# Optimization experiments

Hardware: AMD Instinct MI355X
Metric: run time of the kernel (lower is better)

## Reference

```python
import jax, jax.numpy as jnp
import numpy as np

TILE = 16       # tile_size
R = 8           # search_radius
MAX_OFF = 8     # max initial offset magnitude used in setup
PAD = R + MAX_OFF  # padding so all gathers are in-bounds


def setup_inputs() -> dict:
    key = jax.random.key(0)
    k1, k2, k3 = jax.random.split(key, 3)
    B, C, H, W = 4, 3, 512, 512
    src = jax.random.normal(k1, (B, C, H, W), jnp.float32)
    dst = jax.random.normal(k2, (B, C, H, W), jnp.float32)
    offset = jax.random.randint(k3, (B, 2, H // TILE, W // TILE), 0, 9).astype(jnp.int32)
    return {"src": src, "dst": dst, "offset": offset}


def _gather_patches(img, rows, cols):
    # img: [C, Hp, Wp]; rows/cols: [nTH, nTW, K] -> [C, nTH, nTW, K, K]
    return img[:, rows[:, :, :, None], cols[:, :, None, :]]


def _tile_matching(src, dst, offset, tile=TILE, r=R, pad=PAD):
    B, C, H, W = src.shape
    nTH, nTW = H // tile, W // tile
    win = tile + 2 * r
    nD = 2 * r + 1

    dst_pad = jnp.pad(dst, ((0, 0), (0, 0), (pad, pad), (pad, pad)))
    off_y = offset[:, 0]  # [B, nTH, nTW]
    off_x = offset[:, 1]

    ti = (jnp.arange(nTH) * tile)  # tile origins (rows)
    tj = (jnp.arange(nTW) * tile)  # tile origins (cols)
    ar = jnp.arange(win)

    rows = ti[None, :, None, None] + off_y[..., None] + (pad - r) + ar
    cols = tj[None, None, :, None] + off_x[..., None] + (pad - r) + ar

    patches = jax.vmap(_gather_patches)(dst_pad, rows, cols)

    # Source tiles: [B, C, nTH, nTW, tile, tile]
    src_t = src.reshape(B, C, nTH, tile, nTW, tile).transpose(0, 1, 2, 4, 3, 5)

    def step(carry, d):
        best_c, best_i = carry
        dy, dx = d // nD, d % nD
        cand = jax.lax.dynamic_slice(
            patches, (0, 0, 0, 0, dy, dx), (B, C, nTH, nTW, tile, tile))
        cost = jnp.abs(cand - src_t).sum(axis=(1, 4, 5))  # SAD: [B, nTH, nTW]
        better = cost < best_c
        return (jnp.where(better, cost, best_c),
                jnp.where(better, d, best_i)), None

    init = (jnp.full((B, nTH, nTW), jnp.inf, src.dtype),
            jnp.zeros((B, nTH, nTW), jnp.int32))
    (best_c, best_i), _ = jax.lax.scan(step, init, jnp.arange(nD * nD, dtype=jnp.int32))

    dy = best_i // nD - r  # best displacement in [-r, r]
    dx = best_i % nD - r
    new_off = jnp.stack([off_y + dy, off_x + dx], axis=1)  # [B, 2, nTH, nTW]

    # Gather aligned dst tiles at refined offsets -> aligned image [B, C, H, W]
    art = jnp.arange(tile)
    rows2 = ti[None, :, None, None] + (off_y + dy)[..., None] + pad + art
    cols2 = tj[None, None, :, None] + (off_x + dx)[..., None] + pad + art
    aligned_t = jax.vmap(_gather_patches)(dst_pad, rows2, cols2)
    aligned = aligned_t.transpose(0, 1, 2, 4, 3, 5).reshape(B, C, H, W)
    return new_off, aligned


def reference(src, dst, offset):
    return _tile_matching(src, dst, offset)
```

## Files before the change

### kernel.cpp

```cpp
#include <hip/hip_runtime.h>

#define TILE 16
#define RR 8
#define ND 17
#define HH 512
#define WW 512
#define CC 3
#define BB 4
#define WROWS 32
#define WSTR 36
#define SSTR 20
#define BLK 256

typedef float f4a __attribute__((ext_vector_type(4), aligned(4)));
typedef unsigned long long u64;

template <int N>
__device__ __forceinline__ float shl_add(float x) {
    return x + __int_as_float(
        __builtin_amdgcn_update_dpp(0, __float_as_int(x), 0x100 + N, 0xF, 0xF, true));
}
template <int MASK>
__device__ __forceinline__ float swz_add(float x) {
    int y = __builtin_amdgcn_ds_swizzle(__float_as_int(x), (MASK << 10) | 0x1F);
    return x + __int_as_float(y);
}

__device__ __forceinline__ u64 sad_pass(const float* Wl, const float S[CC][8],
                                        int dy, int i, int h, int jg) {
    float acc[9];
    #pragma unroll
    for (int a = 0; a < 9; ++a) acc[a] = 0.f;
    #pragma unroll
    for (int c = 0; c < CC; ++c) {
        const int wb = c * (WROWS * WSTR) + (dy + i) * WSTR + 8 * (h + jg);
        f4a a0 = *(const f4a*)&Wl[wb + 0];
        f4a a1 = *(const f4a*)&Wl[wb + 4];
        f4a a2 = *(const f4a*)&Wl[wb + 8];
        f4a a3 = *(const f4a*)&Wl[wb + 12];
        float W16[16] = { a0.x, a0.y, a0.z, a0.w, a1.x, a1.y, a1.z, a1.w,
                          a2.x, a2.y, a2.z, a2.w, a3.x, a3.y, a3.z, a3.w };
        #pragma unroll
        for (int a = 0; a < 9; ++a) {
            float s0 = acc[a];
            #pragma unroll
            for (int jl = 0; jl < 8; ++jl)
                s0 += fabsf(W16[a + jl] - S[c][jl]);
            acc[a] = s0;
        }
    }
    #pragma unroll
    for (int a = 0; a < 9; ++a) {
        float x = acc[a];
        x = shl_add<2>(x);
        x = shl_add<4>(x);
        x = shl_add<8>(x);
        x = swz_add<16>(x);
        x += __shfl_xor(x, 32);
        acc[a] = x;
    }
    float bc = h ? acc[1] : acc[0];
    int   ba = h;
    #pragma unroll
    for (int a = 1; a < 9; ++a)
        if (a > h && acc[a] < bc) { bc = acc[a]; ba = a; }
    const unsigned d = (unsigned)(dy * ND + 8 * h + ba);
    u64 key = ((u64)__float_as_uint(bc) << 32) | d;
    u64 ok  = __shfl_xor(key, 1);
    return ok < key ? ok : key;
}

__global__ __launch_bounds__(BLK, 8) void tile_kernel(const float* __restrict__ src,
                                                      const float* __restrict__ dst,
                                                      const int* __restrict__ offset,
                                                      float* __restrict__ out) {
    __shared__ float Wl[CC * WROWS * WSTR];
    __shared__ float Sl[CC * TILE * SSTR];
    __shared__ u64   keyL[4];

    const int bid  = blockIdx.x;
    const int tile = ((bid & 7) << 9) | (bid >> 3);
    const int b  = tile >> 10;
    const int th = (tile >> 5) & 31;
    const int tw = tile & 31;
    const int ti = th * TILE, tj = tw * TILE;
    const int oy = offset[(b * 2 + 0) * 1024 + th * 32 + tw];
    const int ox = offset[(b * 2 + 1) * 1024 + th * 32 + tw];
    const int t  = threadIdx.x;

    const int gy0 = ti + oy - RR;
    const int gx0 = tj + ox - RR;
    for (int k = t; k < CC * WROWS * 8; k += BLK) {
        int c   = k >> 8;
        int rem = k & 255;
        int row = rem >> 3;
        int cc  = (rem & 7) << 2;
        int gy = gy0 + row;
        int gx = gx0 + cc;
        float4 v = make_float4(0.f, 0.f, 0.f, 0.f);
        if ((unsigned)gy < HH) {
            const float* p = dst + ((size_t)(b * CC + c) * HH + gy) * WW;
            if ((unsigned)gx <= WW - 4) {
                f4a u = *(const f4a*)(p + gx);
                v = make_float4(u.x, u.y, u.z, u.w);
            } else {
                float* ve = (float*)&v;
                #pragma unroll
                for (int e = 0; e < 4; ++e) {
                    int g = gx + e;
                    if ((unsigned)g < WW) ve[e] = p[g];
                }
            }
        }
        *(f4a*)&Wl[c * (WROWS * WSTR) + row * WSTR + cc] = *(f4a*)&v;
    }
    if (t < 192) {
        int k   = t;
        int c   = k >> 6;
        int rem = k & 63;
        int row = rem >> 2;
        int cc  = (rem & 3) << 2;
        f4a v = *(const f4a*)(src + ((size_t)(b * CC + c) * HH + ti + row) * WW + tj + cc);
        *(f4a*)&Sl[c * (TILE * SSTR) + row * SSTR + cc] = v;
    }
    __syncthreads();

    const int wv = t >> 6;
    const int l  = t & 63;
    const int h  = l & 1;
    const int jg = (l >> 1) & 1;
    const int i  = l >> 2;

    float S[CC][8];
    #pragma unroll
    for (int c = 0; c < CC; ++c) {
        const int sb = c * (TILE * SSTR) + i * SSTR + 8 * jg;
        f4a s0 = *(const f4a*)&Sl[sb];
        f4a s1 = *(const f4a*)&Sl[sb + 4];
        S[c][0]=s0.x; S[c][1]=s0.y; S[c][2]=s0.z; S[c][3]=s0.w;
        S[c][4]=s1.x; S[c][5]=s1.y; S[c][6]=s1.z; S[c][7]=s1.w;
    }

    u64 bestkey = sad_pass(Wl, S, wv, i, h, jg);
    #pragma unroll
    for (int p = 1; p < 4; ++p) {
        u64 k2 = sad_pass(Wl, S, wv + 4 * p, i, h, jg);
        if (k2 < bestkey) bestkey = k2;
    }
    if (wv == 0) {
        u64 k2 = sad_pass(Wl, S, 16, i, h, jg);
        if (k2 < bestkey) bestkey = k2;
    }
    if (l == 0) keyL[wv] = bestkey;
    __syncthreads();

    u64 wk = keyL[0];
    #pragma unroll
    for (int w = 1; w < 4; ++w) { u64 kw = keyL[w]; if (kw < wk) wk = kw; }
    const int d   = (int)(wk & 0xFFFFFFFFu);
    const int bdy = d / ND;
    const int bdx = d - bdy * ND;

    if (t == 0) out[(b * 2 + 0) * 1024 + th * 32 + tw] = (float)(oy + bdy - RR);
    if (t == 1) out[(b * 2 + 1) * 1024 + th * 32 + tw] = (float)(ox + bdx - RR);

    float* aligned = out + BB * 2 * 1024;
    if (t < 192) {
        const int c   = t >> 6;
        const int rem = t & 63;
        const int ii  = rem >> 2;
        const int jj4 = (rem & 3) << 2;
        const float* wp = &Wl[c * (WROWS * WSTR) + (bdy + ii) * WSTR + bdx + jj4];
        float4 v = make_float4(wp[0], wp[1], wp[2], wp[3]);
        *(f4a*)&aligned[((size_t)(b * CC + c) * HH + ti + ii) * WW + tj + jj4] =
            *(f4a*)&v;
    }
}

extern "C" void kernel_launch(void* const* d_in, const int* in_sizes, int n_in,
                              void* d_out, int out_size, void* d_ws, size_t ws_size,
                              hipStream_t stream) {
    const float* src    = (const float*)d_in[0];
    const float* dst    = (const float*)d_in[1];
    const int*   offset = (const int*)d_in[2];
    float*       out    = (float*)d_out;
    tile_kernel<<<dim3(BB * 1024), BLK, 0, stream>>>(src, dst, offset, out);
}
```

Baseline: 115.3 us.

## Read search window directly from global memory for interior tiles, skipping LDS staging

For tiles whose search window lies fully in-bounds, SAD passes now load dst rows straight from global memory (through the caches) instead of staging the window in LDS. The source tile is also loaded into registers directly from global, removing its LDS buffer. Border tiles keep the LDS path. This drops the staging loads, LDS writes and one barrier, but replaces cheap LDS reads with repeated unaligned global loads that depend on L1/L2 hit rates and add latency.

New measurement: 131.3 us. 1.14x slower.

```diff
diff --git a/kernel.cpp b/kernel.cpp
--- a/kernel.cpp
+++ b/kernel.cpp
@@ -9,7 +9,6 @@
 #define BB 4
 #define WROWS 32
 #define WSTR 36
-#define SSTR 20
 #define BLK 256
 
 typedef float f4a __attribute__((ext_vector_type(4), aligned(4)));
@@ -26,29 +25,21 @@
     return x + __int_as_float(y);
 }
 
-__device__ __forceinline__ u64 sad_pass(const float* Wl, const float S[CC][8],
-                                        int dy, int i, int h, int jg) {
-    float acc[9];
-    #pragma unroll
-    for (int a = 0; a < 9; ++a) acc[a] = 0.f;
-    #pragma unroll
-    for (int c = 0; c < CC; ++c) {
-        const int wb = c * (WROWS * WSTR) + (dy + i) * WSTR + 8 * (h + jg);
-        f4a a0 = *(const f4a*)&Wl[wb + 0];
-        f4a a1 = *(const f4a*)&Wl[wb + 4];
-        f4a a2 = *(const f4a*)&Wl[wb + 8];
-        f4a a3 = *(const f4a*)&Wl[wb + 12];
-        float W16[16] = { a0.x, a0.y, a0.z, a0.w, a1.x, a1.y, a1.z, a1.w,
-                          a2.x, a2.y, a2.z, a2.w, a3.x, a3.y, a3.z, a3.w };
-        #pragma unroll
-        for (int a = 0; a < 9; ++a) {
-            float s0 = acc[a];
-            #pragma unroll
-            for (int jl = 0; jl < 8; ++jl)
-                s0 += fabsf(W16[a + jl] - S[c][jl]);
-            acc[a] = s0;
-        }
-    }
+__device__ __forceinline__ void sad_core(f4a a0, f4a a1, f4a a2, f4a a3,
+                                         const float Sc[8], float (&acc)[9]) {
+    float W16[16] = { a0.x, a0.y, a0.z, a0.w, a1.x, a1.y, a1.z, a1.w,
+                      a2.x, a2.y, a2.z, a2.w, a3.x, a3.y, a3.z, a3.w };
+    #pragma unroll
+    for (int a = 0; a < 9; ++a) {
+        float s0 = acc[a];
+        #pragma unroll
+        for (int jl = 0; jl < 8; ++jl)
+            s0 += fabsf(W16[a + jl] - Sc[jl]);
+        acc[a] = s0;
+    }
+}
+
+__device__ __forceinline__ u64 reduce_key(float (&acc)[9], int dy, int h) {
     #pragma unroll
     for (int a = 0; a < 9; ++a) {
         float x = acc[a];
@@ -70,12 +61,39 @@
     return ok < key ? ok : key;
 }
 
+__device__ __forceinline__ u64 sad_pass_lds(const float* Wl, const float S[CC][8],
+                                            int dy, int i, int h, int jg) {
+    float acc[9];
+    #pragma unroll
+    for (int a = 0; a < 9; ++a) acc[a] = 0.f;
+    #pragma unroll
+    for (int c = 0; c < CC; ++c) {
+        const int wb = c * (WROWS * WSTR) + (dy + i) * WSTR + 8 * (h + jg);
+        sad_core(*(const f4a*)&Wl[wb + 0], *(const f4a*)&Wl[wb + 4],
+                 *(const f4a*)&Wl[wb + 8], *(const f4a*)&Wl[wb + 12], S[c], acc);
+    }
+    return reduce_key(acc, dy, h);
+}
+
+__device__ __forceinline__ u64 sad_pass_glb(const float* wp, const float S[CC][8],
+                                            int dy, int h) {
+    float acc[9];
+    #pragma unroll
+    for (int a = 0; a < 9; ++a) acc[a] = 0.f;
+    #pragma unroll
+    for (int c = 0; c < CC; ++c) {
+        const float* p = wp + ((size_t)(c * HH) + dy) * WW;
+        sad_core(*(const f4a*)(p + 0), *(const f4a*)(p + 4),
+                 *(const f4a*)(p + 8), *(const f4a*)(p + 12), S[c], acc);
+    }
+    return reduce_key(acc, dy, h);
+}
+
 __global__ __launch_bounds__(BLK, 8) void tile_kernel(const float* __restrict__ src,
                                                       const float* __restrict__ dst,
                                                       const int* __restrict__ offset,
                                                       float* __restrict__ out) {
     __shared__ float Wl[CC * WROWS * WSTR];
-    __shared__ float Sl[CC * TILE * SSTR];
     __shared__ u64   keyL[4];
 
     const int bid  = blockIdx.x;
@@ -90,40 +108,8 @@
 
     const int gy0 = ti + oy - RR;
     const int gx0 = tj + ox - RR;
-    for (int k = t; k < CC * WROWS * 8; k += BLK) {
-        int c   = k >> 8;
-        int rem = k & 255;
-        int row = rem >> 3;
-        int cc  = (rem & 7) << 2;
-        int gy = gy0 + row;
-        int gx = gx0 + cc;
-        float4 v = make_float4(0.f, 0.f, 0.f, 0.f);
-        if ((unsigned)gy < HH) {
-            const float* p = dst + ((size_t)(b * CC + c) * HH + gy) * WW;
-            if ((unsigned)gx <= WW - 4) {
-                f4a u = *(const f4a*)(p + gx);
-                v = make_float4(u.x, u.y, u.z, u.w);
-            } else {
-                float* ve = (float*)&v;
-                #pragma unroll
-                for (int e = 0; e < 4; ++e) {
-                    int g = gx + e;
-                    if ((unsigned)g < WW) ve[e] = p[g];
-                }
-            }
-        }
-        *(f4a*)&Wl[c * (WROWS * WSTR) + row * WSTR + cc] = *(f4a*)&v;
-    }
-    if (t < 192) {
-        int k   = t;
-        int c   = k >> 6;
-        int rem = k & 63;
-        int row = rem >> 2;
-        int cc  = (rem & 3) << 2;
-        f4a v = *(const f4a*)(src + ((size_t)(b * CC + c) * HH + ti + row) * WW + tj + cc);
-        *(f4a*)&Sl[c * (TILE * SSTR) + row * SSTR + cc] = v;
-    }
-    __syncthreads();
+    const bool fast = (gy0 >= 0) && (gy0 <= HH - WROWS) &&
+                      (gx0 >= 0) && (gx0 <= WW - WROWS);
 
     const int wv = t >> 6;
     const int l  = t & 63;
@@ -132,25 +118,70 @@
     const int i  = l >> 2;
 
     float S[CC][8];
-    #pragma unroll
-    for (int c = 0; c < CC; ++c) {
-        const int sb = c * (TILE * SSTR) + i * SSTR + 8 * jg;
-        f4a s0 = *(const f4a*)&Sl[sb];
-        f4a s1 = *(const f4a*)&Sl[sb + 4];
-        S[c][0]=s0.x; S[c][1]=s0.y; S[c][2]=s0.z; S[c][3]=s0.w;
-        S[c][4]=s1.x; S[c][5]=s1.y; S[c][6]=s1.z; S[c][7]=s1.w;
-    }
-
-    u64 bestkey = sad_pass(Wl, S, wv, i, h, jg);
-    #pragma unroll
-    for (int p = 1; p < 4; ++p) {
-        u64 k2 = sad_pass(Wl, S, wv + 4 * p, i, h, jg);
-        if (k2 < bestkey) bestkey = k2;
-    }
-    if (wv == 0) {
-        u64 k2 = sad_pass(Wl, S, 16, i, h, jg);
-        if (k2 < bestkey) bestkey = k2;
-    }
+    {
+        const float* sp = src + ((size_t)(b * CC) * HH + ti + i) * WW + tj + 8 * jg;
+        #pragma unroll
+        for (int c = 0; c < CC; ++c) {
+            f4a s0 = *(const f4a*)(sp + (size_t)c * HH * WW);
+            f4a s1 = *(const f4a*)(sp + (size_t)c * HH * WW + 4);
+            S[c][0]=s0.x; S[c][1]=s0.y; S[c][2]=s0.z; S[c][3]=s0.w;
+            S[c][4]=s1.x; S[c][5]=s1.y; S[c][6]=s1.z; S[c][7]=s1.w;
+        }
+    }
+
+    u64 bestkey;
+    if (fast) {
+        const float* wp = dst + ((size_t)(b * CC) * HH + gy0 + i) * WW
+                              + gx0 + 8 * (h + jg);
+        bestkey = sad_pass_glb(wp, S, wv, h);
+        #pragma unroll
+        for (int p = 1; p < 4; ++p) {
+            u64 k2 = sad_pass_glb(wp, S, wv + 4 * p, h);
+            if (k2 < bestkey) bestkey = k2;
+        }
+        if (wv == 0) {
+            u64 k2 = sad_pass_glb(wp, S, 16, h);
+            if (k2 < bestkey) bestkey = k2;
+        }
+    } else {
+        for (int k = t; k < CC * WROWS * 8; k += BLK) {
+            int c   = k >> 8;
+            int rem = k & 255;
+            int row = rem >> 3;
+            int cc  = (rem & 7) << 2;
+            int gy = gy0 + row;
+            int gx = gx0 + cc;
+            float4 v = make_float4(0.f, 0.f, 0.f, 0.f);
+            if ((unsigned)gy < HH) {
+                const float* p = dst + ((size_t)(b * CC + c) * HH + gy) * WW;
+                if ((unsigned)gx <= WW - 4) {
+                    f4a u = *(const f4a*)(p + gx);
+                    v = make_float4(u.x, u.y, u.z, u.w);
+                } else {
+                    float* ve = (float*)&v;
+                    #pragma unroll
+                    for (int e = 0; e < 4; ++e) {
+                        int g = gx + e;
+                        if ((unsigned)g < WW) ve[e] = p[g];
+                    }
+                }
+            }
+            *(f4a*)&Wl[c * (WROWS * WSTR) + row * WSTR + cc] = *(f4a*)&v;
+        }
+        __syncthreads();
+
+        bestkey = sad_pass_lds(Wl, S, wv, i, h, jg);
+        #pragma unroll
+        for (int p = 1; p < 4; ++p) {
+            u64 k2 = sad_pass_lds(Wl, S, wv + 4 * p, i, h, jg);
+            if (k2 < bestkey) bestkey = k2;
+        }
+        if (wv == 0) {
+            u64 k2 = sad_pass_lds(Wl, S, 16, i, h, jg);
+            if (k2 < bestkey) bestkey = k2;
+        }
+    }
+
     if (l == 0) keyL[wv] = bestkey;
     __syncthreads();
 
@@ -170,8 +201,16 @@
         const int rem = t & 63;
         const int ii  = rem >> 2;
         const int jj4 = (rem & 3) << 2;
-        const float* wp = &Wl[c * (WROWS * WSTR) + (bdy + ii) * WSTR + bdx + jj4];
-        float4 v = make_float4(wp[0], wp[1], wp[2], wp[3]);
+        float4 v;
+        if (fast) {
+            const float* gp = dst + ((size_t)(b * CC + c) * HH + gy0 + bdy + ii) * WW
+                                  + gx0 + bdx + jj4;
+            f4a u = *(const f4a*)gp;
+            v = make_float4(u.x, u.y, u.z, u.w);
+        } else {
+            const float* wp = &Wl[c * (WROWS * WSTR) + (bdy + ii) * WSTR + bdx + jj4];
+            v = make_float4(wp[0], wp[1], wp[2], wp[3]);
+        }
         *(f4a*)&aligned[((size_t)(b * CC + c) * HH + ti + ii) * WW + tj + jj4] =
             *(f4a*)&v;
     }
```
